# Performance work log

Hardware: AMD Instinct MI355X
Metric: run time of the kernel (lower is better)

## Reference

```python
import jax, jax.numpy as jnp
import numpy as np

NV = 40962      # icosphere level 6 vertices: 10*4^6 + 2
NF = 81920      # faces: 2*(NV-2)
BS, CIN, COUT, NCOEFF = 8, 32, 64, 4


def _make_sparse(rng, n_rows, n_cols, nnz_per_row, scale):
    rows = np.repeat(np.arange(n_rows, dtype=np.int32), nnz_per_row)
    cols = rng.integers(0, n_cols, size=n_rows * nnz_per_row).astype(np.int32)
    vals = (rng.standard_normal(n_rows * nnz_per_row) * scale).astype(np.float32)
    return jnp.asarray(rows), jnp.asarray(cols), jnp.asarray(vals)


def setup_inputs() -> dict:
    key = jax.random.key(0)
    k_in, k_ew, k_ns, k_co = jax.random.split(key, 4)
    rng = np.random.default_rng(0)

    # G: [3*NF, NV], 3 nnz per row (face gradient from 3 incident vertices)
    G_rows, G_cols, G_vals = _make_sparse(rng, 3 * NF, NV, 3, 0.5)
    # L: [NV, NV], ~7 nnz per row (icosphere Laplacian stencil)
    L_rows, L_cols, L_vals = _make_sparse(rng, NV, NV, 7, 0.3)
    # F2V: [NV, NF], ~6 nnz per row (face-to-vertex averaging)
    F_rows, F_cols, F_vals = _make_sparse(rng, NV, NF, 6, 1.0 / 6.0)

    stdv = 1.0 / np.sqrt(CIN * NCOEFF)
    return {
        "input": jax.random.normal(k_in, (BS, CIN, NV), dtype=jnp.float32),
        "G_rows": G_rows, "G_cols": G_cols, "G_vals": G_vals,
        "L_rows": L_rows, "L_cols": L_cols, "L_vals": L_vals,
        "F_rows": F_rows, "F_cols": F_cols, "F_vals": F_vals,
        "EW": jax.random.normal(k_ew, (NF, 3), dtype=jnp.float32),
        "NS": jax.random.normal(k_ns, (NF, 3), dtype=jnp.float32),
        "coeffs": jax.random.uniform(k_co, (CIN * NCOEFF, COUT), dtype=jnp.float32,
                                     minval=-stdv, maxval=stdv),
        "nv_prev": NV,
        "nf": NF,
    }


def _spmatmul(x, rows, cols, vals, m):
    # x: [bs, c, n]; sparse op S: [m, n] in COO -> out: [bs, c, m]
    gathered = x[:, :, cols] * vals  # [bs, c, nnz]
    return jnp.zeros(x.shape[:2] + (m,), x.dtype).at[:, :, rows].add(gathered)


def reference(input, G_rows, G_cols, G_vals, L_rows, L_cols, L_vals,
              F_rows, F_cols, F_vals, EW, NS, coeffs, nv_prev, nf):
    bs, in_ch, _ = input.shape
    # per-face gradient: [bs, c, 3*nf] -> [bs, c, nf, 3]
    grad_face = _spmatmul(input, G_rows, G_cols, G_vals, 3 * nf)
    grad_face = grad_face.reshape(bs, in_ch, 3, nf).transpose(0, 1, 3, 2)
    laplacian = _spmatmul(input, L_rows, L_cols, L_vals, nv_prev)
    identity = input[..., :nv_prev]
    grad_face_ew = jnp.sum(grad_face * EW, axis=-1)  # [bs, c, nf]
    grad_face_ns = jnp.sum(grad_face * NS, axis=-1)
    grad_vert_ew = _spmatmul(grad_face_ew, F_rows, F_cols, F_vals, nv_prev)
    grad_vert_ns = _spmatmul(grad_face_ns, F_rows, F_cols, F_vals, nv_prev)
    feat = jnp.stack([identity, laplacian, grad_vert_ew, grad_vert_ns], axis=-1)  # [bs,c,nv,4]
    # dense projection; row-major flatten of (c,4) matches torch reshape ordering
    w = coeffs.reshape(in_ch, 4, -1)  # [c, 4, out]
    out = jnp.einsum('bcvk,cko->bov', feat, w)  # [bs, out, nv]  (bias unused in original forward)
    return out
```

## Files before the change

### kernel.cpp

```cpp
#include <hip/hip_runtime.h>

#define NV 40962
#define NF 81920
#define BSZ 8
#define CIN 32
#define COUT 64
#define BC 256

typedef unsigned short u16;
typedef float    f32x4 __attribute__((ext_vector_type(4)));
typedef _Float16 f16x8 __attribute__((ext_vector_type(8)));

__device__ __forceinline__ float bf2f(u16 h) {
    return __uint_as_float(((unsigned int)h) << 16);
}
__device__ __forceinline__ u16 f2bf(float f) {
    unsigned int u = __float_as_uint(f);
    unsigned int r = (u + 0x7fffu + ((u >> 16) & 1u)) >> 16;
    return (u16)r;
}

__global__ __launch_bounds__(256) void k_transpose(const float* __restrict__ in,
                                                   u16* __restrict__ xt) {
    __shared__ float tile[32][33];
    int c0 = blockIdx.x * 32;
    int r0 = blockIdx.y * 32;
    int tx = threadIdx.x & 31;
    int ty = threadIdx.x >> 5;
    #pragma unroll
    for (int i = 0; i < 32; i += 8) {
        int cc = c0 + tx;
        float v = 0.f;
        if (cc < NV) v = in[(size_t)(r0 + ty + i) * NV + cc];
        tile[ty + i][tx] = v;
    }
    __syncthreads();
    int t = threadIdx.x;
    #pragma unroll
    for (int e = t; e < 512; e += 256) {
        int vl = e >> 4;
        int p  = e & 15;
        int v  = c0 + vl;
        if (v < NV) {
            ushort2 val;
            val.x = f2bf(tile[p * 2][vl]);
            val.y = f2bf(tile[p * 2 + 1][vl]);
            *(ushort2*)&xt[(size_t)v * BC + r0 + p * 2] = val;
        }
    }
}

__global__ __launch_bounds__(256) void k_faces(const u16* __restrict__ xt,
                                               const int* __restrict__ Gc,
                                               const float* __restrict__ Gv,
                                               const float* __restrict__ EW,
                                               const float* __restrict__ NS,
                                               u16* __restrict__ gfew,
                                               u16* __restrict__ gfns) {
    int t  = threadIdx.x;
    int f  = blockIdx.x * 2 + (t >> 7);
    int c2 = t & 127;
    float a0ew = 0.f, a1ew = 0.f, a0ns = 0.f, a1ns = 0.f;
    #pragma unroll
    for (int d = 0; d < 3; ++d) {
        int base = 3 * (d * NF + f);
        float g0 = 0.f, g1 = 0.f;
        #pragma unroll
        for (int j = 0; j < 3; ++j) {
            int   col = Gc[base + j];
            float val = Gv[base + j];
            ushort2 xv = *(const ushort2*)&xt[(size_t)col * BC + c2 * 2];
            g0 += val * bf2f(xv.x);
            g1 += val * bf2f(xv.y);
        }
        float ew = EW[f * 3 + d], ns = NS[f * 3 + d];
        a0ew += ew * g0;  a1ew += ew * g1;
        a0ns += ns * g0;  a1ns += ns * g1;
    }
    ushort2 o;
    o.x = f2bf(a0ew); o.y = f2bf(a1ew);
    *(ushort2*)&gfew[(size_t)f * BC + c2 * 2] = o;
    o.x = f2bf(a0ns); o.y = f2bf(a1ns);
    *(ushort2*)&gfns[(size_t)f * BC + c2 * 2] = o;
}

#define VT 8
#define FROW 136
#define FBP  (16 * FROW)

__global__ __launch_bounds__(256, 6) void k_vertices(const u16* __restrict__ xt,
                                                  const int* __restrict__ Lc,
                                                  const float* __restrict__ Lv,
                                                  const int* __restrict__ Fc,
                                                  const float* __restrict__ Fv,
                                                  const u16* __restrict__ gfew,
                                                  const u16* __restrict__ gfns,
                                                  const float* __restrict__ coeffs,
                                                  float* __restrict__ out) {
    __shared__ _Float16 fh[4 * FBP];
    int t = threadIdx.x;

    const int nwg = (NV + VT - 1) / VT;
    const int q = nwg >> 3, r = nwg & 7;
    int orig = blockIdx.x;
    int xcd = orig & 7, lid = orig >> 3;
    int swz = (xcd < r ? xcd * (q + 1) : r * (q + 1) + (xcd - r) * q) + lid;
    int v0 = swz * VT;

    int w  = t >> 6;
    int l  = t & 63;
    int lr = l & 15;
    int lq = l >> 4;
    f16x8 Bh[4], Bl[4];
    #pragma unroll
    for (int ks = 0; ks < 4; ++ks) {
        #pragma unroll
        for (int e = 0; e < 8; ++e) {
            int k = ks * 32 + lq * 8 + e;
            float c = coeffs[k * 64 + w * 16 + lr];
            _Float16 h = (_Float16)c;
            Bh[ks][e] = h;
            Bl[ks][e] = (_Float16)(c - (float)h);
        }
    }

    int p   = t & 127;
    int vh  = __builtin_amdgcn_readfirstlane(t >> 7);
    int b   = p >> 4;
    int c2  = p & 15;
    int bc0 = p * 2;
    int bp  = b >> 1;
    int rbase = (b & 1) * 8;
    #pragma unroll
    for (int vi = 0; vi < 4; ++vi) {
        int vloc = vh * 4 + vi;
        int v = v0 + vloc;
        float id0 = 0.f, id1 = 0.f, lap0 = 0.f, lap1 = 0.f;
        float ew0 = 0.f, ew1 = 0.f, ns0 = 0.f, ns1 = 0.f;
        if (v < NV) {
            ushort2 xv = *(const ushort2*)&(xt + (size_t)v * BC)[bc0];
            ushort2 lt[7];
            float   lw[7];
            #pragma unroll
            for (int j = 0; j < 7; ++j) {
                int col = Lc[7 * v + j];
                lw[j]   = Lv[7 * v + j];
                lt[j]   = *(const ushort2*)&(xt + (size_t)col * BC)[bc0];
            }
            ushort2 et[6], nt[6];
            float   fw6[6];
            #pragma unroll
            for (int j = 0; j < 6; ++j) {
                int col = Fc[6 * v + j];
                fw6[j]  = Fv[6 * v + j];
                et[j]   = *(const ushort2*)&(gfew + (size_t)col * BC)[bc0];
                nt[j]   = *(const ushort2*)&(gfns + (size_t)col * BC)[bc0];
            }
            id0 = bf2f(xv.x);  id1 = bf2f(xv.y);
            #pragma unroll
            for (int j = 0; j < 7; ++j) {
                lap0 += lw[j] * bf2f(lt[j].x);
                lap1 += lw[j] * bf2f(lt[j].y);
            }
            #pragma unroll
            for (int j = 0; j < 6; ++j) {
                ew0 += fw6[j] * bf2f(et[j].x);  ew1 += fw6[j] * bf2f(et[j].y);
                ns0 += fw6[j] * bf2f(nt[j].x);  ns1 += fw6[j] * bf2f(nt[j].y);
            }
        }
        float fv[8] = {id0, lap0, ew0, ns0, id1, lap1, ew1, ns1};
        f16x8 hv;
        #pragma unroll
        for (int e = 0; e < 8; ++e) hv[e] = (_Float16)fv[e];
        int idx = bp * FBP + (rbase + vloc) * FROW + c2 * 8;
        *(f16x8*)&fh[idx] = hv;
    }
    __syncthreads();

    #pragma unroll
    for (int bp2 = 0; bp2 < 4; ++bp2) {
        f32x4 acc = {0.f, 0.f, 0.f, 0.f};
        #pragma unroll
        for (int ks = 0; ks < 4; ++ks) {
            int aidx = bp2 * FBP + lr * FROW + ks * 32 + lq * 8;
            f16x8 A = *(const f16x8*)&fh[aidx];
            acc = __builtin_amdgcn_mfma_f32_16x16x32_f16(A, Bh[ks], acc, 0, 0, 0);
            acc = __builtin_amdgcn_mfma_f32_16x16x32_f16(A, Bl[ks], acc, 0, 0, 0);
        }
        int r0 = lq * 4;
        int bb = bp2 * 2 + (r0 >> 3);
        int vbase = v0 + (r0 & 7);
        int o = w * 16 + lr;
        size_t off = ((size_t)(bb * 64 + o)) * NV + vbase;
        if (v0 + VT <= NV) {
            *(float2*)&out[off]     = make_float2(acc.x, acc.y);
            *(float2*)&out[off + 2] = make_float2(acc.z, acc.w);
        } else {
            #pragma unroll
            for (int j = 0; j < 4; ++j)
                if (vbase + j < NV) out[off + j] = acc[j];
        }
    }
}

extern "C" void kernel_launch(void* const* d_in, const int* in_sizes, int n_in,
                              void* d_out, int out_size, void* d_ws, size_t ws_size,
                              hipStream_t stream) {
    (void)in_sizes; (void)n_in; (void)out_size; (void)ws_size;
    const float* input = (const float*)d_in[0];
    const int*   Gc = (const int*)d_in[2];
    const float* Gv = (const float*)d_in[3];
    const int*   Lc = (const int*)d_in[5];
    const float* Lv = (const float*)d_in[6];
    const int*   Fc = (const int*)d_in[8];
    const float* Fv = (const float*)d_in[9];
    const float* EW = (const float*)d_in[10];
    const float* NS = (const float*)d_in[11];
    const float* coeffs = (const float*)d_in[12];
    float* out = (float*)d_out;

    u16* ws   = (u16*)d_ws;
    u16* xt   = ws;
    u16* gfew = ws + (size_t)NV * BC;
    u16* gfns = gfew + (size_t)NF * BC;

    dim3 gA((NV + 31) / 32, BC / 32);
    k_transpose<<<gA, 256, 0, stream>>>(input, xt);

    k_faces<<<dim3(NF / 2), 256, 0, stream>>>(xt, Gc, Gv, EW, NS, gfew, gfns);

    k_vertices<<<dim3((NV + VT - 1) / VT), 256, 0, stream>>>(
        xt, Lc, Lv, Fc, Fv, gfew, gfns, coeffs, out);
}
```

Baseline: 172.9 us.

## Interleave face gradients, widen per-thread gathers, swizzle LDS feature tile

Face gradient outputs for EW and NS are now interleaved into one buffer, so the vertex kernel fetches both with a single 16-byte load per face instead of two 4-byte loads. Both the face and vertex kernels now handle 4 channels per thread with 8-byte gathers, and all index/weight loads are issued before the dependent gathers. The LDS feature tile gets an XOR swizzle to cut bank conflicts on the MFMA A reads, and vertex occupancy hint drops from 6 to 4 waves. Wider loads raise register pressure and halve the threads per gather row.

```diff
diff --git a/kernel.cpp b/kernel.cpp
--- a/kernel.cpp
+++ b/kernel.cpp
@@ -10,6 +10,8 @@
 typedef unsigned short u16;
 typedef float    f32x4 __attribute__((ext_vector_type(4)));
 typedef _Float16 f16x8 __attribute__((ext_vector_type(8)));
+typedef unsigned short u16x4 __attribute__((ext_vector_type(4)));
+typedef unsigned short u16x8 __attribute__((ext_vector_type(8)));
 
 __device__ __forceinline__ float bf2f(u16 h) {
     return __uint_as_float(((unsigned int)h) << 16);
@@ -55,46 +57,61 @@
                                                const float* __restrict__ Gv,
                                                const float* __restrict__ EW,
                                                const float* __restrict__ NS,
-                                               u16* __restrict__ gfew,
-                                               u16* __restrict__ gfns) {
+                                               u16* __restrict__ gfi) {
     int t  = threadIdx.x;
-    int f  = blockIdx.x * 2 + (t >> 7);
-    int c2 = t & 127;
-    float a0ew = 0.f, a1ew = 0.f, a0ns = 0.f, a1ns = 0.f;
+    int f  = blockIdx.x * 4 + (t >> 6);
+    int p4 = t & 63;
+    int bc0 = p4 * 4;
+
+    int   gc[9]; float gv[9];
+    #pragma unroll
+    for (int i = 0; i < 9; ++i) {
+        int d = i / 3, j = i - d * 3;
+        int base = 3 * (d * NF + f) + j;
+        gc[i] = Gc[base];
+        gv[i] = Gv[base];
+    }
+    float ewd[3], nsd[3];
+    #pragma unroll
+    for (int d = 0; d < 3; ++d) { ewd[d] = EW[f * 3 + d]; nsd[d] = NS[f * 3 + d]; }
+
+    u16x4 xr[9];
+    #pragma unroll
+    for (int i = 0; i < 9; ++i)
+        xr[i] = *(const u16x4*)&xt[(size_t)gc[i] * BC + bc0];
+
+    float aew[4] = {0.f, 0.f, 0.f, 0.f}, ans[4] = {0.f, 0.f, 0.f, 0.f};
     #pragma unroll
     for (int d = 0; d < 3; ++d) {
-        int base = 3 * (d * NF + f);
-        float g0 = 0.f, g1 = 0.f;
+        float g[4] = {0.f, 0.f, 0.f, 0.f};
         #pragma unroll
         for (int j = 0; j < 3; ++j) {
-            int   col = Gc[base + j];
-            float val = Gv[base + j];
-            ushort2 xv = *(const ushort2*)&xt[(size_t)col * BC + c2 * 2];
-            g0 += val * bf2f(xv.x);
-            g1 += val * bf2f(xv.y);
-        }
-        float ew = EW[f * 3 + d], ns = NS[f * 3 + d];
-        a0ew += ew * g0;  a1ew += ew * g1;
-        a0ns += ns * g0;  a1ns += ns * g1;
-    }
-    ushort2 o;
-    o.x = f2bf(a0ew); o.y = f2bf(a1ew);
-    *(ushort2*)&gfew[(size_t)f * BC + c2 * 2] = o;
-    o.x = f2bf(a0ns); o.y = f2bf(a1ns);
-    *(ushort2*)&gfns[(size_t)f * BC + c2 * 2] = o;
+            float val = gv[d * 3 + j];
+            #pragma unroll
+            for (int k = 0; k < 4; ++k) g[k] += val * bf2f(xr[d * 3 + j][k]);
+        }
+        #pragma unroll
+        for (int k = 0; k < 4; ++k) {
+            aew[k] += ewd[d] * g[k];
+            ans[k] += nsd[d] * g[k];
+        }
+    }
+    u16x8 o;
+    o[0] = f2bf(aew[0]); o[1] = f2bf(aew[1]); o[2] = f2bf(ans[0]); o[3] = f2bf(ans[1]);
+    o[4] = f2bf(aew[2]); o[5] = f2bf(aew[3]); o[6] = f2bf(ans[2]); o[7] = f2bf(ans[3]);
+    *(u16x8*)&gfi[(size_t)f * 512 + p4 * 8] = o;
 }
 
 #define VT 8
 #define FROW 136
 #define FBP  (16 * FROW)
 
-__global__ __launch_bounds__(256, 6) void k_vertices(const u16* __restrict__ xt,
+__global__ __launch_bounds__(256, 4) void k_vertices(const u16* __restrict__ xt,
                                                   const int* __restrict__ Lc,
                                                   const float* __restrict__ Lv,
                                                   const int* __restrict__ Fc,
                                                   const float* __restrict__ Fv,
-                                                  const u16* __restrict__ gfew,
-                                                  const u16* __restrict__ gfns,
+                                                  const u16* __restrict__ gfi,
                                                   const float* __restrict__ coeffs,
                                                   float* __restrict__ out) {
     __shared__ _Float16 fh[4 * FBP];
@@ -107,7 +124,63 @@
     int swz = (xcd < r ? xcd * (q + 1) : r * (q + 1) + (xcd - r) * q) + lid;
     int v0 = swz * VT;
 
-    int w  = t >> 6;
+    int p4 = t & 63;
+    int vg = t >> 6;
+    int b  = p4 >> 3;
+    int c4 = p4 & 7;
+    int bc0 = p4 * 4;
+    int bp = b >> 1;
+    int rbase = (b & 1) * 8;
+    int bkey = (b & 3) << 4;
+
+    for (int vi = 0; vi < 2; ++vi) {
+        int vloc = vg * 2 + vi;
+        int v = v0 + vloc;
+        float id[4]  = {0.f,0.f,0.f,0.f}, lp[4] = {0.f,0.f,0.f,0.f};
+        float ew[4]  = {0.f,0.f,0.f,0.f}, ns[4] = {0.f,0.f,0.f,0.f};
+        if (v < NV) {
+            int   lc[7]; float lwv[7];
+            #pragma unroll
+            for (int j = 0; j < 7; ++j) { lc[j] = Lc[7 * v + j]; lwv[j] = Lv[7 * v + j]; }
+            int   fc[6]; float fwv[6];
+            #pragma unroll
+            for (int j = 0; j < 6; ++j) { fc[j] = Fc[6 * v + j]; fwv[j] = Fv[6 * v + j]; }
+            u16x4 xv = *(const u16x4*)&xt[(size_t)v * BC + bc0];
+            u16x4 lt[7];
+            #pragma unroll
+            for (int j = 0; j < 7; ++j)
+                lt[j] = *(const u16x4*)&xt[(size_t)lc[j] * BC + bc0];
+            u16x8 ft[6];
+            #pragma unroll
+            for (int j = 0; j < 6; ++j)
+                ft[j] = *(const u16x8*)&gfi[(size_t)fc[j] * 512 + p4 * 8];
+            #pragma unroll
+            for (int k = 0; k < 4; ++k) id[k] = bf2f(xv[k]);
+            #pragma unroll
+            for (int j = 0; j < 7; ++j)
+                #pragma unroll
+                for (int k = 0; k < 4; ++k) lp[k] += lwv[j] * bf2f(lt[j][k]);
+            #pragma unroll
+            for (int j = 0; j < 6; ++j) {
+                float val = fwv[j];
+                ew[0] += val * bf2f(ft[j][0]);  ew[1] += val * bf2f(ft[j][1]);
+                ns[0] += val * bf2f(ft[j][2]);  ns[1] += val * bf2f(ft[j][3]);
+                ew[2] += val * bf2f(ft[j][4]);  ew[3] += val * bf2f(ft[j][5]);
+                ns[2] += val * bf2f(ft[j][6]);  ns[3] += val * bf2f(ft[j][7]);
+            }
+        }
+        int row = rbase + vloc;
+        int rowsh = bp * FBP + row * FROW;
+        f16x8 h0, h1;
+        h0[0]=(_Float16)id[0]; h0[1]=(_Float16)lp[0]; h0[2]=(_Float16)ew[0]; h0[3]=(_Float16)ns[0];
+        h0[4]=(_Float16)id[1]; h0[5]=(_Float16)lp[1]; h0[6]=(_Float16)ew[1]; h0[7]=(_Float16)ns[1];
+        h1[0]=(_Float16)id[2]; h1[1]=(_Float16)lp[2]; h1[2]=(_Float16)ew[2]; h1[3]=(_Float16)ns[2];
+        h1[4]=(_Float16)id[3]; h1[5]=(_Float16)lp[3]; h1[6]=(_Float16)ew[3]; h1[7]=(_Float16)ns[3];
+        *(f16x8*)&fh[rowsh + (((c4 * 32)      ^ bkey) >> 1)] = h0;
+        *(f16x8*)&fh[rowsh + (((c4 * 32 + 16) ^ bkey) >> 1)] = h1;
+    }
+
+    int w  = vg;
     int l  = t & 63;
     int lr = l & 15;
     int lq = l >> 4;
@@ -123,67 +196,16 @@
             Bl[ks][e] = (_Float16)(c - (float)h);
         }
     }
-
-    int p   = t & 127;
-    int vh  = __builtin_amdgcn_readfirstlane(t >> 7);
-    int b   = p >> 4;
-    int c2  = p & 15;
-    int bc0 = p * 2;
-    int bp  = b >> 1;
-    int rbase = (b & 1) * 8;
-    #pragma unroll
-    for (int vi = 0; vi < 4; ++vi) {
-        int vloc = vh * 4 + vi;
-        int v = v0 + vloc;
-        float id0 = 0.f, id1 = 0.f, lap0 = 0.f, lap1 = 0.f;
-        float ew0 = 0.f, ew1 = 0.f, ns0 = 0.f, ns1 = 0.f;
-        if (v < NV) {
-            ushort2 xv = *(const ushort2*)&(xt + (size_t)v * BC)[bc0];
-            ushort2 lt[7];
-            float   lw[7];
-            #pragma unroll
-            for (int j = 0; j < 7; ++j) {
-                int col = Lc[7 * v + j];
-                lw[j]   = Lv[7 * v + j];
-                lt[j]   = *(const ushort2*)&(xt + (size_t)col * BC)[bc0];
-            }
-            ushort2 et[6], nt[6];
-            float   fw6[6];
-            #pragma unroll
-            for (int j = 0; j < 6; ++j) {
-                int col = Fc[6 * v + j];
-                fw6[j]  = Fv[6 * v + j];
-                et[j]   = *(const ushort2*)&(gfew + (size_t)col * BC)[bc0];
-                nt[j]   = *(const ushort2*)&(gfns + (size_t)col * BC)[bc0];
-            }
-            id0 = bf2f(xv.x);  id1 = bf2f(xv.y);
-            #pragma unroll
-            for (int j = 0; j < 7; ++j) {
-                lap0 += lw[j] * bf2f(lt[j].x);
-                lap1 += lw[j] * bf2f(lt[j].y);
-            }
-            #pragma unroll
-            for (int j = 0; j < 6; ++j) {
-                ew0 += fw6[j] * bf2f(et[j].x);  ew1 += fw6[j] * bf2f(et[j].y);
-                ns0 += fw6[j] * bf2f(nt[j].x);  ns1 += fw6[j] * bf2f(nt[j].y);
-            }
-        }
-        float fv[8] = {id0, lap0, ew0, ns0, id1, lap1, ew1, ns1};
-        f16x8 hv;
-        #pragma unroll
-        for (int e = 0; e < 8; ++e) hv[e] = (_Float16)fv[e];
-        int idx = bp * FBP + (rbase + vloc) * FROW + c2 * 8;
-        *(f16x8*)&fh[idx] = hv;
-    }
     __syncthreads();
 
     #pragma unroll
     for (int bp2 = 0; bp2 < 4; ++bp2) {
+        int akey = ((bp2 * 2 + (lr >> 3)) & 3) << 4;
         f32x4 acc = {0.f, 0.f, 0.f, 0.f};
         #pragma unroll
         for (int ks = 0; ks < 4; ++ks) {
-            int aidx = bp2 * FBP + lr * FROW + ks * 32 + lq * 8;
-            f16x8 A = *(const f16x8*)&fh[aidx];
+            int byteoff = (ks * 64 + lq * 16) ^ akey;
+            f16x8 A = *(const f16x8*)&fh[bp2 * FBP + lr * FROW + (byteoff >> 1)];
             acc = __builtin_amdgcn_mfma_f32_16x16x32_f16(A, Bh[ks], acc, 0, 0, 0);
             acc = __builtin_amdgcn_mfma_f32_16x16x32_f16(A, Bl[ks], acc, 0, 0, 0);
         }
@@ -219,16 +241,15 @@
     const float* coeffs = (const float*)d_in[12];
     float* out = (float*)d_out;
 
-    u16* ws   = (u16*)d_ws;
-    u16* xt   = ws;
-    u16* gfew = ws + (size_t)NV * BC;
-    u16* gfns = gfew + (size_t)NF * BC;
+    u16* ws  = (u16*)d_ws;
+    u16* xt  = ws;
+    u16* gfi = ws + (size_t)NV * BC;
 
     dim3 gA((NV + 31) / 32, BC / 32);
     k_transpose<<<gA, 256, 0, stream>>>(input, xt);
 
-    k_faces<<<dim3(NF / 2), 256, 0, stream>>>(xt, Gc, Gv, EW, NS, gfew, gfns);
+    k_faces<<<dim3(NF / 4), 256, 0, stream>>>(xt, Gc, Gv, EW, NS, gfi);
 
     k_vertices<<<dim3((NV + VT - 1) / VT), 256, 0, stream>>>(
-        xt, Lc, Lv, Fc, Fv, gfew, gfns, coeffs, out);
-}
+        xt, Lc, Lv, Fc, Fv, gfi, coeffs, out);
+}
```

Result: faster. 151.0 us (-12.7%).
